# Kernel tuning notes

Hardware: AMD Instinct MI355X
Metric: run time of the kernel (lower is better)

The kernel has to match this reference:

```python
import jax, jax.numpy as jnp
import numpy as np

SCALE = 0.2  # scale init arg, clipped to [0,1]


def _relative_corners(rank):
    # [2**rank, rank] matrix of +-1 corner coordinates
    return jnp.array([[float(int(c)) * 2.0 - 1.0 for c in format(i, '0%db' % rank)]
                      for i in range(2 ** rank)], dtype=jnp.float32)


def _affine_from_noise(random_u):
    # random_u: [B, 2**r, r] uniform(0,1) -> random_scale uniform(1-SCALE, 1)
    B, n, r = random_u.shape
    out_c = _relative_corners(r)                                  # [2^r, r]
    random_scale = (1.0 - SCALE) + SCALE * random_u
    src = out_c[None] * random_scale                              # [B, 2^r, r]
    ones_col = jnp.ones((B, n, 1), jnp.float32)
    A = jnp.broadcast_to(
        jnp.concatenate([out_c, jnp.ones((n, 1), jnp.float32)], -1)[None],
        (B, n, r + 1))                                            # output corners (homog.)
    Bmat = jnp.concatenate([src, ones_col], -1)                   # source corners (homog.)
    # least-squares solve A X = B  (matrix_solve_ls): X = (A^T A)^{-1} A^T B
    AtA = jnp.einsum('bni,bnj->bij', A, A)
    AtB = jnp.einsum('bni,bnj->bij', A, Bmat)
    X = jnp.linalg.solve(AtA, AtB)                                # [B, r+1, r+1]
    return jnp.transpose(X, (0, 2, 1))                            # transform, [B, r+1, r+1]


def _make_grid(transform, spatial_shape):
    # AffineGridWarper: output voxel coords normalized to [-1,1], affine-mapped,
    # then converted to source pixel coordinates [0, size-1].
    r = len(spatial_shape)
    axes = [jnp.linspace(-1.0, 1.0, s) for s in spatial_shape]
    mesh = jnp.stack(jnp.meshgrid(*axes, indexing='ij'), -1)      # [D,H,W,r]
    mesh_h = jnp.concatenate(
        [mesh, jnp.ones(tuple(spatial_shape) + (1,), jnp.float32)], -1)
    coords = jnp.einsum('dhwj,bij->bdhwi', mesh_h, transform[:, :r, :])  # [B,D,H,W,r]
    sizes = jnp.array(spatial_shape, jnp.float32)
    return (coords + 1.0) * (sizes - 1.0) * 0.5                   # pixel coords


def _resample_linear_zero(img, coords):
    # trilinear interpolation with zero boundary: out-of-range corners contribute 0
    # img: [B,D,H,W,C], coords: [B,D,H,W,3] (pixel coordinates)
    B = img.shape[0]
    sp = jnp.array(img.shape[1:4], jnp.int32)
    f = jnp.floor(coords)
    frac = coords - f                                             # [B,D,H,W,3]
    i0 = f.astype(jnp.int32)
    bidx = jnp.arange(B)[:, None, None, None]
    out = jnp.zeros(img.shape, img.dtype)
    for corner in range(8):  # fixed structural loop over 2^3 interpolation corners
        off = jnp.array([(corner >> 2) & 1, (corner >> 1) & 1, corner & 1], jnp.int32)
        idx = i0 + off
        valid = jnp.all((idx >= 0) & (idx < sp), axis=-1)         # [B,D,H,W]
        ci = jnp.clip(idx, 0, sp - 1)
        vals = img[bidx, ci[..., 0], ci[..., 1], ci[..., 2]]      # [B,D,H,W,C]
        w = jnp.prod(jnp.where(off == 1, frac, 1.0 - frac), axis=-1)
        w = w * valid.astype(img.dtype)
        out = out + vals * w[..., None]
    return out


def setup_inputs() -> dict:
    key = jax.random.key(0)
    k1, k2 = jax.random.split(key)
    input_tensor = jax.random.normal(k1, (8, 128, 128, 128, 1), dtype=jnp.float32)
    random_u = jax.random.uniform(k2, (8, 8, 3), dtype=jnp.float32)
    return {"input_tensor": input_tensor, "random_u": random_u}


def reference(input_tensor, random_u):
    transform = _affine_from_noise(random_u)                      # [B,4,4]
    grid = _make_grid(transform, input_tensor.shape[1:4])         # [B,D,H,W,3]
    return _resample_linear_zero(input_tensor, grid)
```

## Files before the change

kernel.cpp:

```cpp
#include <hip/hip_runtime.h>

#define NB   8
#define NS   128
#define VOX  (NS*NS*NS)

#define DS_D  11
#define DS_H  15
#define ROW_W 40

typedef __attribute__((address_space(1))) const void gconst_t;
typedef __attribute__((address_space(3))) void lds_t;

__global__ __launch_bounds__(256) void warp_resample_kernel(
        const float* __restrict__ img, const float* __restrict__ u,
        float* __restrict__ out) {
    __shared__ __align__(16) float tm[12];
    __shared__ __align__(16) float slab[DS_D * DS_H * ROW_W + 8];

    const int tid  = threadIdx.x;
    const int bi   = blockIdx.x;
    const int wblk =  bi       & 3;
    const int hblk = (bi >> 2) & 15;
    const int dblk = (bi >> 6) & 31;
    const int b    =  bi >> 11;

    if (tid < 12) {
        int i = tid >> 2, j = tid & 3;
        float acc = 0.f;
#pragma unroll
        for (int n = 0; n < 8; ++n) {
            float ci = (n & (4 >> i)) ? 1.f : -1.f;
            float cj = (j < 3) ? ((n & (4 >> j)) ? 1.f : -1.f) : 1.f;
            float s  = 0.8f + 0.2f * u[(b * 8 + n) * 3 + i];
            acc += cj * ci * s;
        }
        tm[tid] = acc * 0.125f;
    }
    __syncthreads();

    const float4 T0 = *(const float4*)&tm[0];
    const float4 T1 = *(const float4*)&tm[4];
    const float4 T2 = *(const float4*)&tm[8];

    const int d0 = dblk << 2, h0 = hblk << 3, w0 = wblk << 5;
    const float inv = 2.0f / 127.0f;
    const float x0 = -1.f + d0 * inv, y0 = -1.f + h0 * inv, z0 = -1.f + w0 * inv;
    const float P0 = (T0.x * x0 + T0.y * y0 + T0.z * z0 + T0.w + 1.f) * 63.5f;
    const float P1 = (T1.x * x0 + T1.y * y0 + T1.z * z0 + T1.w + 1.f) * 63.5f;
    const float P2 = (T2.x * x0 + T2.y * y0 + T2.z * z0 + T2.w + 1.f) * 63.5f;

    float mn0 = P0 + fminf(0.f, 3.f*T0.x) + fminf(0.f, 7.f*T0.y) + fminf(0.f, 31.f*T0.z);
    float mx0 = P0 + fmaxf(0.f, 3.f*T0.x) + fmaxf(0.f, 7.f*T0.y) + fmaxf(0.f, 31.f*T0.z);
    float mn1 = P1 + fminf(0.f, 3.f*T1.x) + fminf(0.f, 7.f*T1.y) + fminf(0.f, 31.f*T1.z);
    float mx1 = P1 + fmaxf(0.f, 3.f*T1.x) + fmaxf(0.f, 7.f*T1.y) + fmaxf(0.f, 31.f*T1.z);
    float mn2 = P2 + fminf(0.f, 3.f*T2.x) + fminf(0.f, 7.f*T2.y) + fminf(0.f, 31.f*T2.z);
    float mx2 = P2 + fmaxf(0.f, 3.f*T2.x) + fmaxf(0.f, 7.f*T2.y) + fmaxf(0.f, 31.f*T2.z);

    const int i0mn = (int)floorf(mn0), i0mx = (int)floorf(mx0);
    const int i1mn = (int)floorf(mn1), i1mx = (int)floorf(mx1);
    const int i2mn = (int)floorf(mn2), i2mx = (int)floorf(mx2);

    const int d_lo = min(max(i0mn - 1, 0), NS - 1);
    const int d_hi = min(max(i0mx + 2, 0), NS - 1);
    const int h_lo = min(max(i1mn - 1, 0), NS - 1);
    const int h_hi = min(max(i1mx + 2, 0), NS - 1);
    const int Sd   = min(d_hi - d_lo + 1, DS_D);
    const int Sh   = min(h_hi - h_lo + 1, DS_H);
    const int ws   = min(max((i2mn - 1) & ~3, 0), NS - ROW_W);

    const bool interior = (i0mn >= 1) && (i0mx <= 125) &&
                          (i1mn >= 1) && (i1mx <= 125) &&
                          (i2mn >= 1) && (i2mx <= 125);

    {
        const float* gb = img + (size_t)b * VOX;
        int hi = tid / 10;
        int c  = tid - hi * 10;
        bool active = (hi < Sh);
        int wvbase = (tid & ~63) << 2;
        for (int di = 0; di < Sd; ++di) {
            if (active) {
                const float* g = gb + (((d_lo + di) * NS + (h_lo + hi)) * NS + ws + (c << 2));
                __builtin_amdgcn_global_load_lds(
                    (gconst_t*)g,
                    (lds_t*)(slab + di * Sh * ROW_W + wvbase),
                    16, 0, 0);
            }
        }
    }
    __syncthreads();

    const int wg = tid & 7, hh = (tid >> 3) & 7, dd = tid >> 6;
    const int d = d0 + dd, h = h0 + hh, wbase = w0 + (wg << 2);

    float q0 = P0 + dd * T0.x + hh * T0.y + (float)(wg << 2) * T0.z;
    float q1 = P1 + dd * T1.x + hh * T1.y + (float)(wg << 2) * T1.z;
    float q2 = P2 + dd * T2.x + hh * T2.y + (float)(wg << 2) * T2.z;

    const int rstride = Sh * ROW_W;
    float res[4];

    if (interior) {
#pragma unroll
        for (int k = 0; k < 4; ++k) {
            float f0 = floorf(q0), f1 = floorf(q1), f2 = floorf(q2);
            int   i0 = (int)f0,    i1 = (int)f1,    i2 = (int)f2;
            float r0 = q0 - f0,    r1 = q1 - f1,    r2 = q2 - f2;

            int base = (i0 - d_lo) * rstride + (i1 - h_lo) * ROW_W + (i2 - ws);
            float a00 = slab[base],              b00 = slab[base + 1];
            float a01 = slab[base + ROW_W],      b01 = slab[base + ROW_W + 1];
            int base2 = base + rstride;
            float a10 = slab[base2],             b10 = slab[base2 + 1];
            float a11 = slab[base2 + ROW_W],     b11 = slab[base2 + ROW_W + 1];

            float e0 = fmaf(r2, b00 - a00, a00);
            float e1 = fmaf(r2, b01 - a01, a01);
            float e2 = fmaf(r2, b10 - a10, a10);
            float e3 = fmaf(r2, b11 - a11, a11);
            float c0 = fmaf(r1, e1 - e0, e0);
            float c1 = fmaf(r1, e3 - e2, e2);
            res[k] = fmaf(r0, c1 - c0, c0);

            q0 += T0.z; q1 += T1.z; q2 += T2.z;
        }
    } else {
#pragma unroll
        for (int k = 0; k < 4; ++k) {
            float f0 = floorf(q0), f1 = floorf(q1), f2 = floorf(q2);
            int   i0 = (int)f0,    i1 = (int)f1,    i2 = (int)f2;
            float r0 = q0 - f0,    r1 = q1 - f1,    r2 = q2 - f2;

            float wd0 = (i0 >= 0     && i0 < NS)     ? (1.0f - r0) : 0.0f;
            float wd1 = (i0 + 1 < NS)                ? r0          : 0.0f;
            float wh0 = (i1 >= 0     && i1 < NS)     ? (1.0f - r1) : 0.0f;
            float wh1 = (i1 + 1 < NS)                ? r1          : 0.0f;
            float ww0 = (i2 >= 0     && i2 < NS)     ? (1.0f - r2) : 0.0f;
            float ww1 = (i2 + 1 >= 0 && i2 + 1 < NS) ? r2          : 0.0f;

            int cw0 = min(max(i2,     0), NS - 1);
            int cw1 = min(max(i2 + 1, 0), NS - 1);
            int dI0 = min(max(min(max(i0,     0), NS - 1) - d_lo, 0), Sd - 1);
            int dI1 = min(max(min(max(i0 + 1, 0), NS - 1) - d_lo, 0), Sd - 1);
            int hI0 = min(max(min(max(i1,     0), NS - 1) - h_lo, 0), Sh - 1);
            int hI1 = min(max(min(max(i1 + 1, 0), NS - 1) - h_lo, 0), Sh - 1);
            int j0  = min(max(cw0 - ws, 0), ROW_W - 1);
            bool same = (cw1 == cw0);

            float acc = 0.f;
            {
                int bb = dI0 * rstride + hI0 * ROW_W + j0;
                float a = slab[bb], bv = slab[bb + 1];
                float rt = same ? a : bv;
                acc = fmaf(fmaf(a, ww0, rt * ww1), wd0 * wh0, acc);
            }
            {
                int bb = dI0 * rstride + hI1 * ROW_W + j0;
                float a = slab[bb], bv = slab[bb + 1];
                float rt = same ? a : bv;
                acc = fmaf(fmaf(a, ww0, rt * ww1), wd0 * wh1, acc);
            }
            {
                int bb = dI1 * rstride + hI0 * ROW_W + j0;
                float a = slab[bb], bv = slab[bb + 1];
                float rt = same ? a : bv;
                acc = fmaf(fmaf(a, ww0, rt * ww1), wd1 * wh0, acc);
            }
            {
                int bb = dI1 * rstride + hI1 * ROW_W + j0;
                float a = slab[bb], bv = slab[bb + 1];
                float rt = same ? a : bv;
                acc = fmaf(fmaf(a, ww0, rt * ww1), wd1 * wh1, acc);
            }
            res[k] = acc;

            q0 += T0.z; q1 += T1.z; q2 += T2.z;
        }
    }

    size_t oidx = (((size_t)(b * NS + d) * NS + h) * NS) + wbase;
    *reinterpret_cast<float4*>(out + oidx) =
        make_float4(res[0], res[1], res[2], res[3]);
}

extern "C" void kernel_launch(void* const* d_in, const int* in_sizes, int n_in,
                              void* d_out, int out_size, void* d_ws, size_t ws_size,
                              hipStream_t stream) {
    const float* img = (const float*)d_in[0];
    const float* u   = (const float*)d_in[1];
    float* out = (float*)d_out;

    int blocks = NB * 32 * 16 * 4;
    warp_resample_kernel<<<blocks, 256, 0, stream>>>(img, u, out);
}
```

Before: 130.7 us.

## Enlarge tile to 8x8x32 with fixed-size slab and depth-walking threads

Each block now covers 8 depth slices instead of 4, so the block count halves and the staged LDS slab (fixed 14x14x40) is shared by more outputs, which cuts redundant halo loads from global memory. Each thread owns one w coordinate and steps through 8 depth slices, writing scalar coalesced stores per slice instead of one float4. The slab extent is now fixed, so the load loop is fully unrolled, and the base offset and interior flag become wave-uniform via readfirstlane. The larger slab raises LDS use per block, which may lower occupancy, and the interior test is relaxed to rely on the fixed slab bounds.

After: 134.6 us. 3.0% more time.

```diff
diff --git a/kernel.cpp b/kernel.cpp
--- a/kernel.cpp
+++ b/kernel.cpp
@@ -4,9 +4,10 @@
 #define NS   128
 #define VOX  (NS*NS*NS)
 
-#define DS_D  11
-#define DS_H  15
+#define SD    14
+#define SH    14
 #define ROW_W 40
+#define RST   (SH*ROW_W)
 
 typedef __attribute__((address_space(1))) const void gconst_t;
 typedef __attribute__((address_space(3))) void lds_t;
@@ -14,15 +15,15 @@
 __global__ __launch_bounds__(256) void warp_resample_kernel(
         const float* __restrict__ img, const float* __restrict__ u,
         float* __restrict__ out) {
-    __shared__ __align__(16) float tm[12];
-    __shared__ __align__(16) float slab[DS_D * DS_H * ROW_W + 8];
+    __shared__ float tm[12];
+    __shared__ __align__(16) float slab[SD * RST];
 
     const int tid  = threadIdx.x;
     const int bi   = blockIdx.x;
     const int wblk =  bi       & 3;
     const int hblk = (bi >> 2) & 15;
-    const int dblk = (bi >> 6) & 31;
-    const int b    =  bi >> 11;
+    const int dblk = (bi >> 6) & 15;
+    const int b    =  bi >> 10;
 
     if (tid < 12) {
         int i = tid >> 2, j = tid & 3;
@@ -38,81 +39,75 @@
     }
     __syncthreads();
 
-    const float4 T0 = *(const float4*)&tm[0];
-    const float4 T1 = *(const float4*)&tm[4];
-    const float4 T2 = *(const float4*)&tm[8];
+    const float t00 = tm[0], t01 = tm[1], t02 = tm[2],  t03 = tm[3];
+    const float t10 = tm[4], t11 = tm[5], t12 = tm[6],  t13 = tm[7];
+    const float t20 = tm[8], t21 = tm[9], t22 = tm[10], t23 = tm[11];
 
-    const int d0 = dblk << 2, h0 = hblk << 3, w0 = wblk << 5;
+    const int d0 = dblk << 3, h0 = hblk << 3, w0 = wblk << 5;
     const float inv = 2.0f / 127.0f;
     const float x0 = -1.f + d0 * inv, y0 = -1.f + h0 * inv, z0 = -1.f + w0 * inv;
-    const float P0 = (T0.x * x0 + T0.y * y0 + T0.z * z0 + T0.w + 1.f) * 63.5f;
-    const float P1 = (T1.x * x0 + T1.y * y0 + T1.z * z0 + T1.w + 1.f) * 63.5f;
-    const float P2 = (T2.x * x0 + T2.y * y0 + T2.z * z0 + T2.w + 1.f) * 63.5f;
+    const float P0 = (t00 * x0 + t01 * y0 + t02 * z0 + t03 + 1.f) * 63.5f;
+    const float P1 = (t10 * x0 + t11 * y0 + t12 * z0 + t13 + 1.f) * 63.5f;
+    const float P2 = (t20 * x0 + t21 * y0 + t22 * z0 + t23 + 1.f) * 63.5f;
 
-    float mn0 = P0 + fminf(0.f, 3.f*T0.x) + fminf(0.f, 7.f*T0.y) + fminf(0.f, 31.f*T0.z);
-    float mx0 = P0 + fmaxf(0.f, 3.f*T0.x) + fmaxf(0.f, 7.f*T0.y) + fmaxf(0.f, 31.f*T0.z);
-    float mn1 = P1 + fminf(0.f, 3.f*T1.x) + fminf(0.f, 7.f*T1.y) + fminf(0.f, 31.f*T1.z);
-    float mx1 = P1 + fmaxf(0.f, 3.f*T1.x) + fmaxf(0.f, 7.f*T1.y) + fmaxf(0.f, 31.f*T1.z);
-    float mn2 = P2 + fminf(0.f, 3.f*T2.x) + fminf(0.f, 7.f*T2.y) + fminf(0.f, 31.f*T2.z);
-    float mx2 = P2 + fmaxf(0.f, 3.f*T2.x) + fmaxf(0.f, 7.f*T2.y) + fmaxf(0.f, 31.f*T2.z);
+    const float mn0 = P0 + fminf(0.f, 7.f*t00) + fminf(0.f, 7.f*t01) + fminf(0.f, 31.f*t02);
+    const float mx0 = P0 + fmaxf(0.f, 7.f*t00) + fmaxf(0.f, 7.f*t01) + fmaxf(0.f, 31.f*t02);
+    const float mn1 = P1 + fminf(0.f, 7.f*t10) + fminf(0.f, 7.f*t11) + fminf(0.f, 31.f*t12);
+    const float mx1 = P1 + fmaxf(0.f, 7.f*t10) + fmaxf(0.f, 7.f*t11) + fmaxf(0.f, 31.f*t12);
+    const float mn2 = P2 + fminf(0.f, 7.f*t20) + fminf(0.f, 7.f*t21) + fminf(0.f, 31.f*t22);
+    const float mx2 = P2 + fmaxf(0.f, 7.f*t20) + fmaxf(0.f, 7.f*t21) + fmaxf(0.f, 31.f*t22);
 
     const int i0mn = (int)floorf(mn0), i0mx = (int)floorf(mx0);
     const int i1mn = (int)floorf(mn1), i1mx = (int)floorf(mx1);
     const int i2mn = (int)floorf(mn2), i2mx = (int)floorf(mx2);
 
-    const int d_lo = min(max(i0mn - 1, 0), NS - 1);
-    const int d_hi = min(max(i0mx + 2, 0), NS - 1);
-    const int h_lo = min(max(i1mn - 1, 0), NS - 1);
-    const int h_hi = min(max(i1mx + 2, 0), NS - 1);
-    const int Sd   = min(d_hi - d_lo + 1, DS_D);
-    const int Sh   = min(h_hi - h_lo + 1, DS_H);
-    const int ws   = min(max((i2mn - 1) & ~3, 0), NS - ROW_W);
+    const int d_lo = min(max(i0mn - 1, 0), NS - SD);
+    const int h_lo = min(max(i1mn - 1, 0), NS - SH);
+    const int ws   = min(max(i2mn - 1, 0) & ~3, NS - ROW_W);
 
-    const bool interior = (i0mn >= 1) && (i0mx <= 125) &&
-                          (i1mn >= 1) && (i1mx <= 125) &&
-                          (i2mn >= 1) && (i2mx <= 125);
+    const int interior = __builtin_amdgcn_readfirstlane(
+        (i0mn >= 0 && i0mx <= 126 && i1mn >= 0 && i1mx <= 126 &&
+         i2mn >= 0 && i2mx <= 126) ? 1 : 0);
+    const int off = __builtin_amdgcn_readfirstlane(
+        -(d_lo * RST + h_lo * ROW_W + ws));
 
     {
         const float* gb = img + (size_t)b * VOX;
-        int hi = tid / 10;
-        int c  = tid - hi * 10;
-        bool active = (hi < Sh);
-        int wvbase = (tid & ~63) << 2;
-        for (int di = 0; di < Sd; ++di) {
-            if (active) {
-                const float* g = gb + (((d_lo + di) * NS + (h_lo + hi)) * NS + ws + (c << 2));
+        const int hi = tid / 10;
+        const int c  = tid - hi * 10;
+        const int wvbase = (tid & ~63) << 2;
+        if (tid < SH * 10) {
+#pragma unroll
+            for (int di = 0; di < SD; ++di) {
+                const float* g = gb + (((d_lo + di) * NS + (h_lo + hi)) * NS
+                                       + ws + (c << 2));
                 __builtin_amdgcn_global_load_lds(
-                    (gconst_t*)g,
-                    (lds_t*)(slab + di * Sh * ROW_W + wvbase),
-                    16, 0, 0);
+                    (gconst_t*)g, (lds_t*)(slab + di * RST + wvbase), 16, 0, 0);
             }
         }
     }
     __syncthreads();
 
-    const int wg = tid & 7, hh = (tid >> 3) & 7, dd = tid >> 6;
-    const int d = d0 + dd, h = h0 + hh, wbase = w0 + (wg << 2);
+    const int wl = tid & 31, hh = tid >> 5;
+    float q0 = P0 + hh * t01 + wl * t02;
+    float q1 = P1 + hh * t11 + wl * t12;
+    float q2 = P2 + hh * t21 + wl * t22;
 
-    float q0 = P0 + dd * T0.x + hh * T0.y + (float)(wg << 2) * T0.z;
-    float q1 = P1 + dd * T1.x + hh * T1.y + (float)(wg << 2) * T1.z;
-    float q2 = P2 + dd * T2.x + hh * T2.y + (float)(wg << 2) * T2.z;
-
-    const int rstride = Sh * ROW_W;
-    float res[4];
+    float res[8];
 
     if (interior) {
 #pragma unroll
-        for (int k = 0; k < 4; ++k) {
+        for (int k = 0; k < 8; ++k) {
             float f0 = floorf(q0), f1 = floorf(q1), f2 = floorf(q2);
             int   i0 = (int)f0,    i1 = (int)f1,    i2 = (int)f2;
             float r0 = q0 - f0,    r1 = q1 - f1,    r2 = q2 - f2;
 
-            int base = (i0 - d_lo) * rstride + (i1 - h_lo) * ROW_W + (i2 - ws);
-            float a00 = slab[base],              b00 = slab[base + 1];
-            float a01 = slab[base + ROW_W],      b01 = slab[base + ROW_W + 1];
-            int base2 = base + rstride;
-            float a10 = slab[base2],             b10 = slab[base2 + 1];
-            float a11 = slab[base2 + ROW_W],     b11 = slab[base2 + ROW_W + 1];
+            int base = i0 * RST + i1 * ROW_W + i2 + off;
+            float a00 = slab[base],           b00 = slab[base + 1];
+            float a01 = slab[base + ROW_W],   b01 = slab[base + ROW_W + 1];
+            int base2 = base + RST;
+            float a10 = slab[base2],          b10 = slab[base2 + 1];
+            float a11 = slab[base2 + ROW_W],  b11 = slab[base2 + ROW_W + 1];
 
             float e0 = fmaf(r2, b00 - a00, a00);
             float e1 = fmaf(r2, b01 - a01, a01);
@@ -122,65 +117,66 @@
             float c1 = fmaf(r1, e3 - e2, e2);
             res[k] = fmaf(r0, c1 - c0, c0);
 
-            q0 += T0.z; q1 += T1.z; q2 += T2.z;
+            q0 += t00; q1 += t10; q2 += t20;
         }
     } else {
 #pragma unroll
-        for (int k = 0; k < 4; ++k) {
+        for (int k = 0; k < 8; ++k) {
             float f0 = floorf(q0), f1 = floorf(q1), f2 = floorf(q2);
             int   i0 = (int)f0,    i1 = (int)f1,    i2 = (int)f2;
             float r0 = q0 - f0,    r1 = q1 - f1,    r2 = q2 - f2;
 
             float wd0 = (i0 >= 0     && i0 < NS)     ? (1.0f - r0) : 0.0f;
-            float wd1 = (i0 + 1 < NS)                ? r0          : 0.0f;
+            float wd1 = (i0 + 1 >= 0 && i0 + 1 < NS) ? r0          : 0.0f;
             float wh0 = (i1 >= 0     && i1 < NS)     ? (1.0f - r1) : 0.0f;
-            float wh1 = (i1 + 1 < NS)                ? r1          : 0.0f;
+            float wh1 = (i1 + 1 >= 0 && i1 + 1 < NS) ? r1          : 0.0f;
             float ww0 = (i2 >= 0     && i2 < NS)     ? (1.0f - r2) : 0.0f;
             float ww1 = (i2 + 1 >= 0 && i2 + 1 < NS) ? r2          : 0.0f;
 
+            int dI0 = min(max(min(max(i0,     0), NS - 1) - d_lo, 0), SD - 1);
+            int dI1 = min(max(min(max(i0 + 1, 0), NS - 1) - d_lo, 0), SD - 1);
+            int hI0 = min(max(min(max(i1,     0), NS - 1) - h_lo, 0), SH - 1);
+            int hI1 = min(max(min(max(i1 + 1, 0), NS - 1) - h_lo, 0), SH - 1);
             int cw0 = min(max(i2,     0), NS - 1);
             int cw1 = min(max(i2 + 1, 0), NS - 1);
-            int dI0 = min(max(min(max(i0,     0), NS - 1) - d_lo, 0), Sd - 1);
-            int dI1 = min(max(min(max(i0 + 1, 0), NS - 1) - d_lo, 0), Sd - 1);
-            int hI0 = min(max(min(max(i1,     0), NS - 1) - h_lo, 0), Sh - 1);
-            int hI1 = min(max(min(max(i1 + 1, 0), NS - 1) - h_lo, 0), Sh - 1);
             int j0  = min(max(cw0 - ws, 0), ROW_W - 1);
             bool same = (cw1 == cw0);
 
             float acc = 0.f;
             {
-                int bb = dI0 * rstride + hI0 * ROW_W + j0;
+                int bb = dI0 * RST + hI0 * ROW_W + j0;
                 float a = slab[bb], bv = slab[bb + 1];
                 float rt = same ? a : bv;
                 acc = fmaf(fmaf(a, ww0, rt * ww1), wd0 * wh0, acc);
             }
             {
-                int bb = dI0 * rstride + hI1 * ROW_W + j0;
+                int bb = dI0 * RST + hI1 * ROW_W + j0;
                 float a = slab[bb], bv = slab[bb + 1];
                 float rt = same ? a : bv;
                 acc = fmaf(fmaf(a, ww0, rt * ww1), wd0 * wh1, acc);
             }
             {
-                int bb = dI1 * rstride + hI0 * ROW_W + j0;
+                int bb = dI1 * RST + hI0 * ROW_W + j0;
                 float a = slab[bb], bv = slab[bb + 1];
                 float rt = same ? a : bv;
                 acc = fmaf(fmaf(a, ww0, rt * ww1), wd1 * wh0, acc);
             }
             {
-                int bb = dI1 * rstride + hI1 * ROW_W + j0;
+                int bb = dI1 * RST + hI1 * ROW_W + j0;
                 float a = slab[bb], bv = slab[bb + 1];
                 float rt = same ? a : bv;
                 acc = fmaf(fmaf(a, ww0, rt * ww1), wd1 * wh1, acc);
             }
             res[k] = acc;
 
-            q0 += T0.z; q1 += T1.z; q2 += T2.z;
+            q0 += t00; q1 += t10; q2 += t20;
         }
     }
 
-    size_t oidx = (((size_t)(b * NS + d) * NS + h) * NS) + wbase;
-    *reinterpret_cast<float4*>(out + oidx) =
-        make_float4(res[0], res[1], res[2], res[3]);
+    size_t ob = (((size_t)(b * NS + d0) * NS + (h0 + hh)) * NS) + w0 + wl;
+#pragma unroll
+    for (int k = 0; k < 8; ++k)
+        out[ob + (size_t)k * NS * NS] = res[k];
 }
 
 extern "C" void kernel_launch(void* const* d_in, const int* in_sizes, int n_in,
@@ -190,6 +186,6 @@
     const float* u   = (const float*)d_in[1];
     float* out = (float*)d_out;
 
-    int blocks = NB * 32 * 16 * 4;
+    int blocks = NB * 16 * 16 * 4;
     warp_resample_kernel<<<blocks, 256, 0, stream>>>(img, u, out);
 }
```
